# Kernel optimization log

Measured on AMD Instinct MI355X. Metric: run time of the kernel, lower is better.

The kernel has to match this reference:

```python
import jax, jax.numpy as jnp
import numpy as np

NSITES, NYEARS, NVIS, HDIM = 100000, 20, 2, 64

def setup_inputs() -> dict:
    key = jax.random.key(0)
    ks = jax.random.split(key, 8)
    # covariates in [-1, 1] as in the original Uniform(-1, 1) sampling
    sxy = jax.random.uniform(ks[0], (NSITES, NYEARS, 2), jnp.float32, -1.0, 1.0)
    oxy = jax.random.uniform(ks[1], (NSITES, NYEARS, NVIS), jnp.float32, -1.0, 1.0)
    p = jnp.zeros((NSITES, NYEARS, NVIS), jnp.float32)
    # Linear params, PyTorch-style fan-in scaled uniform init
    def lin(k, out_f, in_f):
        bound = 1.0 / np.sqrt(in_f)
        kw, kb = jax.random.split(k)
        W = jax.random.uniform(kw, (out_f, in_f), jnp.float32, -bound, bound)
        b = jax.random.uniform(kb, (out_f,), jnp.float32, -bound, bound)
        return W, b
    W_h, b_h = lin(ks[2], HDIM, 2)
    W_psi, b_psi = lin(ks[3], 1, HDIM)
    W_p, b_p = lin(ks[4], 1, HDIM + 1)
    return {"sxy": sxy, "oxy": oxy, "p": p, "W_h": W_h, "b_h": b_h,
            "W_psi": W_psi, "b_psi": b_psi, "W_p": W_p, "b_p": b_p}


def reference(sxy, oxy, p, W_h, b_h, W_psi, b_psi, W_p, b_p):
    # h_out = elu(to_h(sxy))  -> [sites, years, HDIM]
    h = jax.nn.elu(jnp.einsum('syc,hc->syh', sxy, W_h) + b_h)
    # psi_out = sigmoid(to_psi(h)) -> [sites, years, 1]
    psi = jax.nn.sigmoid(jnp.einsum('syh,oh->syo', h, W_psi) + b_psi)
    # to_p(cat(h[s,y], oxy[s,y,v])) decomposed: h part broadcast over visits + scalar covariate term
    w_hpart = W_p[0, :HDIM]   # [HDIM]
    w_x = W_p[0, HDIM]        # scalar weight for the detection covariate
    logit = jnp.einsum('syh,h->sy', h, w_hpart)[:, :, None] + oxy * w_x + b_p[0]
    p_out = jax.nn.sigmoid(logit)  # [sites, years, visits]
    return psi, p_out
```

## Files before the change

kernel.cpp:

```cpp
#include <hip/hip_runtime.h>

#define HDIM  64
#define NPAIR 2000000
#define NVEC  (NPAIR / 2)
#define PVEC  4
#define NT    (NVEC / PVEC)
#define BLOCK 256
#define GRID  ((NT + BLOCK - 1) / BLOCK)

__device__ __forceinline__ float fast_sigmoid(float x) {
    return __builtin_amdgcn_rcpf(1.0f + __expf(-x));
}

__global__ __launch_bounds__(BLOCK) void fused_net(
    const float4* __restrict__ sxy,
    const float4* __restrict__ oxy,
    const float*  __restrict__ W_h,
    const float*  __restrict__ b_h,
    const float*  __restrict__ W_psi,
    const float*  __restrict__ b_psi,
    const float*  __restrict__ W_p,
    const float*  __restrict__ b_p,
    float2* __restrict__ out_psi,
    float4* __restrict__ out_p)
{
    __shared__ __align__(16) float sA[HDIM];
    __shared__ __align__(16) float sB[HDIM];
    __shared__ __align__(16) float sC[HDIM];
    __shared__ __align__(16) float sPsi[HDIM];
    __shared__ __align__(16) float sWp[HDIM];
    __shared__ float sScal[3];

    const int t = threadIdx.x;
    if (t < HDIM) {
        sA[t]   = W_h[2 * t];
        sB[t]   = W_h[2 * t + 1];
        sC[t]   = b_h[t];
        sPsi[t] = W_psi[t];
        sWp[t]  = W_p[t];
    }
    if (t == 0) {
        sScal[0] = b_psi[0];
        sScal[1] = W_p[HDIM];
        sScal[2] = b_p[0];
    }
    __syncthreads();

    const int tid = blockIdx.x * BLOCK + t;
    if (tid >= NT) return;

    const float bpsi = sScal[0];
    const float wx   = sScal[1];
    const float bp   = sScal[2];

    float4 s[PVEC];
#pragma unroll
    for (int k = 0; k < PVEC; ++k) s[k] = sxy[tid + k * NT];

    float psiacc[2 * PVEC], hdacc[2 * PVEC];
#pragma unroll
    for (int j = 0; j < 2 * PVEC; ++j) { psiacc[j] = 0.0f; hdacc[j] = 0.0f; }

    const float4* A4 = reinterpret_cast<const float4*>(sA);
    const float4* B4 = reinterpret_cast<const float4*>(sB);
    const float4* C4 = reinterpret_cast<const float4*>(sC);
    const float4* P4 = reinterpret_cast<const float4*>(sPsi);
    const float4* Q4 = reinterpret_cast<const float4*>(sWp);

#pragma unroll 2
    for (int hq = 0; hq < HDIM / 4; ++hq) {
        const float4 a4 = A4[hq];
        const float4 b4 = B4[hq];
        const float4 c4 = C4[hq];
        const float4 p4 = P4[hq];
        const float4 q4 = Q4[hq];
        const float* af = reinterpret_cast<const float*>(&a4);
        const float* bf = reinterpret_cast<const float*>(&b4);
        const float* cf = reinterpret_cast<const float*>(&c4);
        const float* pf = reinterpret_cast<const float*>(&p4);
        const float* qf = reinterpret_cast<const float*>(&q4);
#pragma unroll
        for (int i = 0; i < 4; ++i) {
            const float a = af[i], b = bf[i], c = cf[i];
            const float wpsi = pf[i], wp = qf[i];
#pragma unroll
            for (int k = 0; k < PVEC; ++k) {
                float z0 = fmaf(a, s[k].x, fmaf(b, s[k].y, c));
                float z1 = fmaf(a, s[k].z, fmaf(b, s[k].w, c));
                float e0 = (z0 > 0.0f) ? z0 : (__expf(z0) - 1.0f);
                float e1 = (z1 > 0.0f) ? z1 : (__expf(z1) - 1.0f);
                psiacc[2 * k]     = fmaf(e0, wpsi, psiacc[2 * k]);
                psiacc[2 * k + 1] = fmaf(e1, wpsi, psiacc[2 * k + 1]);
                hdacc[2 * k]      = fmaf(e0, wp, hdacc[2 * k]);
                hdacc[2 * k + 1]  = fmaf(e1, wp, hdacc[2 * k + 1]);
            }
        }
    }

#pragma unroll
    for (int k = 0; k < PVEC; ++k) {
        const int v = tid + k * NT;
        float2 psi;
        psi.x = fast_sigmoid(psiacc[2 * k] + bpsi);
        psi.y = fast_sigmoid(psiacc[2 * k + 1] + bpsi);
        out_psi[v] = psi;

        const float4 o4 = oxy[v];
        const float l0 = hdacc[2 * k] + bp;
        const float l1 = hdacc[2 * k + 1] + bp;
        float4 p;
        p.x = fast_sigmoid(fmaf(o4.x, wx, l0));
        p.y = fast_sigmoid(fmaf(o4.y, wx, l0));
        p.z = fast_sigmoid(fmaf(o4.z, wx, l1));
        p.w = fast_sigmoid(fmaf(o4.w, wx, l1));
        out_p[v] = p;
    }
}

extern "C" void kernel_launch(void* const* d_in, const int* in_sizes, int n_in,
                              void* d_out, int out_size, void* d_ws, size_t ws_size,
                              hipStream_t stream) {
    const float* sxy   = (const float*)d_in[0];
    const float* oxy   = (const float*)d_in[1];
    const float* W_h   = (const float*)d_in[3];
    const float* b_h   = (const float*)d_in[4];
    const float* W_psi = (const float*)d_in[5];
    const float* b_psi = (const float*)d_in[6];
    const float* W_p   = (const float*)d_in[7];
    const float* b_p   = (const float*)d_in[8];

    float* out = (float*)d_out;
    fused_net<<<GRID, BLOCK, 0, stream>>>(
        (const float4*)sxy, (const float4*)oxy,
        W_h, b_h, W_psi, b_psi, W_p, b_p,
        (float2*)out, (float4*)(out + NPAIR));
}
```

Measured before the change: 128.2 us.

## Use packed FP32 math for hidden-layer loop and read weights from global scalars

Rewrites the per-element hidden-unit loop to use 2-wide vector types so the FMAs can map to packed FP32 instructions. The exponentials now go through exp2 with a pre-scaled argument. Shared-memory staging of the weights and the barrier are removed; weights are read directly from global memory as uniform scalar loads. The pairs per thread drop from 4 to 2 and an occupancy hint is added. This targets VALU instruction count in a compute-bound kernel, at the risk that the weight loads become scalar memory traffic inside the loop and that the compiler does not emit the packed ops.

```diff
diff --git a/kernel.cpp b/kernel.cpp
--- a/kernel.cpp
+++ b/kernel.cpp
@@ -3,16 +3,56 @@
 #define HDIM  64
 #define NPAIR 2000000
 #define NVEC  (NPAIR / 2)
-#define PVEC  4
+#define PVEC  2
 #define NT    (NVEC / PVEC)
 #define BLOCK 256
 #define GRID  ((NT + BLOCK - 1) / BLOCK)
 
-__device__ __forceinline__ float fast_sigmoid(float x) {
-    return __builtin_amdgcn_rcpf(1.0f + __expf(-x));
+typedef float v2f __attribute__((ext_vector_type(2)));
+
+#if __has_builtin(__builtin_elementwise_fma)
+__device__ __forceinline__ v2f pkfma(v2f a, v2f b, v2f c) {
+    return __builtin_elementwise_fma(a, b, c);
+}
+#else
+__device__ __forceinline__ v2f pkfma(v2f a, v2f b, v2f c) {
+    v2f r; r.x = fmaf(a.x, b.x, c.x); r.y = fmaf(a.y, b.y, c.y); return r;
+}
+#endif
+
+#if __has_builtin(__builtin_amdgcn_exp2f)
+#define EXP2(x) __builtin_amdgcn_exp2f(x)
+#else
+#define EXP2(x) exp2f(x)
+#endif
+
+#define LOG2E 1.44269504088896340736f
+
+__device__ __forceinline__ v2f elu2(v2f z) {
+    v2f t = z * LOG2E;
+    v2f e;
+    e.x = EXP2(t.x);
+    e.y = EXP2(t.y);
+    v2f em1 = e + (v2f)(-1.0f);
+    v2f r;
+    r.x = z.x > 0.0f ? z.x : em1.x;
+    r.y = z.y > 0.0f ? z.y : em1.y;
+    return r;
 }
 
-__global__ __launch_bounds__(BLOCK) void fused_net(
+__device__ __forceinline__ v2f sigmoid2(v2f x) {
+    v2f t = x * (-LOG2E);
+    v2f e;
+    e.x = EXP2(t.x);
+    e.y = EXP2(t.y);
+    v2f d = e + (v2f)(1.0f);
+    v2f r;
+    r.x = __builtin_amdgcn_rcpf(d.x);
+    r.y = __builtin_amdgcn_rcpf(d.y);
+    return r;
+}
+
+__global__ __launch_bounds__(BLOCK, 8) void fused_net(
     const float4* __restrict__ sxy,
     const float4* __restrict__ oxy,
     const float*  __restrict__ W_h,
@@ -24,96 +64,63 @@
     float2* __restrict__ out_psi,
     float4* __restrict__ out_p)
 {
-    __shared__ __align__(16) float sA[HDIM];
-    __shared__ __align__(16) float sB[HDIM];
-    __shared__ __align__(16) float sC[HDIM];
-    __shared__ __align__(16) float sPsi[HDIM];
-    __shared__ __align__(16) float sWp[HDIM];
-    __shared__ float sScal[3];
-
-    const int t = threadIdx.x;
-    if (t < HDIM) {
-        sA[t]   = W_h[2 * t];
-        sB[t]   = W_h[2 * t + 1];
-        sC[t]   = b_h[t];
-        sPsi[t] = W_psi[t];
-        sWp[t]  = W_p[t];
-    }
-    if (t == 0) {
-        sScal[0] = b_psi[0];
-        sScal[1] = W_p[HDIM];
-        sScal[2] = b_p[0];
-    }
-    __syncthreads();
-
-    const int tid = blockIdx.x * BLOCK + t;
+    const int tid = blockIdx.x * BLOCK + threadIdx.x;
     if (tid >= NT) return;
 
-    const float bpsi = sScal[0];
-    const float wx   = sScal[1];
-    const float bp   = sScal[2];
+    const float bpsi = b_psi[0];
+    const float wx   = W_p[HDIM];
+    const float bp   = b_p[0];
 
-    float4 s[PVEC];
-#pragma unroll
-    for (int k = 0; k < PVEC; ++k) s[k] = sxy[tid + k * NT];
+    const float4 s0 = sxy[tid];
+    const float4 s1 = sxy[tid + NT];
+    const v2f xs0 = {s0.x, s0.z}, ys0 = {s0.y, s0.w};
+    const v2f xs1 = {s1.x, s1.z}, ys1 = {s1.y, s1.w};
 
-    float psiacc[2 * PVEC], hdacc[2 * PVEC];
-#pragma unroll
-    for (int j = 0; j < 2 * PVEC; ++j) { psiacc[j] = 0.0f; hdacc[j] = 0.0f; }
+    v2f psi0 = (v2f)0.0f, psi1 = (v2f)0.0f;
+    v2f hd0  = (v2f)0.0f, hd1  = (v2f)0.0f;
 
-    const float4* A4 = reinterpret_cast<const float4*>(sA);
-    const float4* B4 = reinterpret_cast<const float4*>(sB);
-    const float4* C4 = reinterpret_cast<const float4*>(sC);
-    const float4* P4 = reinterpret_cast<const float4*>(sPsi);
-    const float4* Q4 = reinterpret_cast<const float4*>(sWp);
+#pragma unroll 8
+    for (int h = 0; h < HDIM; ++h) {
+        const float a    = W_h[2 * h];
+        const float b    = W_h[2 * h + 1];
+        const float c    = b_h[h];
+        const float wpsi = W_psi[h];
+        const float wp   = W_p[h];
 
-#pragma unroll 2
-    for (int hq = 0; hq < HDIM / 4; ++hq) {
-        const float4 a4 = A4[hq];
-        const float4 b4 = B4[hq];
-        const float4 c4 = C4[hq];
-        const float4 p4 = P4[hq];
-        const float4 q4 = Q4[hq];
-        const float* af = reinterpret_cast<const float*>(&a4);
-        const float* bf = reinterpret_cast<const float*>(&b4);
-        const float* cf = reinterpret_cast<const float*>(&c4);
-        const float* pf = reinterpret_cast<const float*>(&p4);
-        const float* qf = reinterpret_cast<const float*>(&q4);
-#pragma unroll
-        for (int i = 0; i < 4; ++i) {
-            const float a = af[i], b = bf[i], c = cf[i];
-            const float wpsi = pf[i], wp = qf[i];
-#pragma unroll
-            for (int k = 0; k < PVEC; ++k) {
-                float z0 = fmaf(a, s[k].x, fmaf(b, s[k].y, c));
-                float z1 = fmaf(a, s[k].z, fmaf(b, s[k].w, c));
-                float e0 = (z0 > 0.0f) ? z0 : (__expf(z0) - 1.0f);
-                float e1 = (z1 > 0.0f) ? z1 : (__expf(z1) - 1.0f);
-                psiacc[2 * k]     = fmaf(e0, wpsi, psiacc[2 * k]);
-                psiacc[2 * k + 1] = fmaf(e1, wpsi, psiacc[2 * k + 1]);
-                hdacc[2 * k]      = fmaf(e0, wp, hdacc[2 * k]);
-                hdacc[2 * k + 1]  = fmaf(e1, wp, hdacc[2 * k + 1]);
-            }
-        }
+        const v2f av = {a, a}, bv = {b, b}, cv = {c, c};
+        const v2f z0 = pkfma(xs0, av, pkfma(ys0, bv, cv));
+        const v2f z1 = pkfma(xs1, av, pkfma(ys1, bv, cv));
+        const v2f e0 = elu2(z0);
+        const v2f e1 = elu2(z1);
+
+        const v2f wpsiv = {wpsi, wpsi}, wpv = {wp, wp};
+        psi0 = pkfma(e0, wpsiv, psi0);
+        psi1 = pkfma(e1, wpsiv, psi1);
+        hd0  = pkfma(e0, wpv, hd0);
+        hd1  = pkfma(e1, wpv, hd1);
     }
 
-#pragma unroll
-    for (int k = 0; k < PVEC; ++k) {
-        const int v = tid + k * NT;
-        float2 psi;
-        psi.x = fast_sigmoid(psiacc[2 * k] + bpsi);
-        psi.y = fast_sigmoid(psiacc[2 * k + 1] + bpsi);
-        out_psi[v] = psi;
+    {
+        const v2f lpsi0 = psi0 + (v2f)bpsi;
+        const v2f lpsi1 = psi1 + (v2f)bpsi;
+        const v2f r0 = sigmoid2(lpsi0);
+        const v2f r1 = sigmoid2(lpsi1);
+        out_psi[tid]      = make_float2(r0.x, r0.y);
+        out_psi[tid + NT] = make_float2(r1.x, r1.y);
 
-        const float4 o4 = oxy[v];
-        const float l0 = hdacc[2 * k] + bp;
-        const float l1 = hdacc[2 * k + 1] + bp;
-        float4 p;
-        p.x = fast_sigmoid(fmaf(o4.x, wx, l0));
-        p.y = fast_sigmoid(fmaf(o4.y, wx, l0));
-        p.z = fast_sigmoid(fmaf(o4.z, wx, l1));
-        p.w = fast_sigmoid(fmaf(o4.w, wx, l1));
-        out_p[v] = p;
+        const float4 o0 = oxy[tid];
+        const float4 o1 = oxy[tid + NT];
+        const v2f wxv = {wx, wx};
+        v2f la = pkfma((v2f){o0.x, o0.y}, wxv, (v2f){hd0.x + bp, hd0.x + bp});
+        v2f lb = pkfma((v2f){o0.z, o0.w}, wxv, (v2f){hd0.y + bp, hd0.y + bp});
+        v2f lc = pkfma((v2f){o1.x, o1.y}, wxv, (v2f){hd1.x + bp, hd1.x + bp});
+        v2f ld = pkfma((v2f){o1.z, o1.w}, wxv, (v2f){hd1.y + bp, hd1.y + bp});
+        const v2f pa = sigmoid2(la);
+        const v2f pb = sigmoid2(lb);
+        const v2f pc = sigmoid2(lc);
+        const v2f pd = sigmoid2(ld);
+        out_p[tid]      = make_float4(pa.x, pa.y, pb.x, pb.y);
+        out_p[tid + NT] = make_float4(pc.x, pc.y, pd.x, pd.y);
     }
 }
 
```

After: 125.3 us. -2.3%, faster.
